# Performance work log

Hardware: AMD Instinct MI355X
Metric: run time of the kernel (lower is better)

Reference implementation:

```python
import jax, jax.numpy as jnp
import numpy as np

GRID_X, GRID_Y, GRID_Z = 200, 200, 8  # grid_size init kwarg (static)


def setup_inputs() -> dict:
    key = jax.random.key(0)
    k1, k2 = jax.random.split(key)
    B, N, D, H, W, C = 4, 6, 41, 16, 44, 64
    # ego-frame points roughly covering the grid extent [-50,50]x[-50,50]x[-4,4]
    scale = jnp.array([55.0, 55.0, 5.0], dtype=jnp.float32)
    geometry = jax.random.uniform(k1, (B, N, D, H, W, 3), dtype=jnp.float32,
                                  minval=-1.0, maxval=1.0) * scale
    features = jax.random.normal(k2, (B, N, D, H, W, C), dtype=jnp.float32)
    voxel_size = jnp.array([0.5, 0.5, 1.0], dtype=jnp.float32)
    voxel_origin = jnp.array([-50.0, -50.0, -4.0], dtype=jnp.float32)
    return {"geometry": geometry, "features": features,
            "voxel_size": voxel_size, "voxel_origin": voxel_origin}


def reference(geometry, features, voxel_size, voxel_origin):
    B = features.shape[0]
    C = features.shape[-1]
    pts = geometry.reshape(B, -1, 3)          # [B, P, 3]
    feat = features.reshape(B, -1, C)         # [B, P, C]

    # metric -> voxel index
    vi = jnp.floor((pts - voxel_origin) / voxel_size).astype(jnp.int32)  # [B, P, 3]
    x, y, z = vi[..., 0], vi[..., 1], vi[..., 2]
    valid = ((x >= 0) & (x < GRID_X) &
             (y >= 0) & (y < GRID_Y) &
             (z >= 0) & (z < GRID_Z))         # [B, P]

    # linear voxel index (z, x, y) ordering; invalid points scatter zeros to slot 0
    lin = z * (GRID_X * GRID_Y) + x * GRID_Y + y
    lin = jnp.where(valid, lin, 0)
    feat_m = jnp.where(valid[..., None], feat, 0.0)

    num_vox = GRID_Z * GRID_X * GRID_Y

    def pool_one(lin_b, feat_b):
        # scatter-add features into dense voxel grid: [num_vox, C]
        return jax.ops.segment_sum(feat_b, lin_b, num_segments=num_vox)

    vox = jax.vmap(pool_one)(lin, feat_m)                         # [B, num_vox, C]
    vox = vox.reshape(B, GRID_Z, GRID_X, GRID_Y, C)
    # torch.cat over z along channel dim => [B, Z*C, X, Y] with z-major blocks
    bev = jnp.transpose(vox, (0, 1, 4, 2, 3)).reshape(B, GRID_Z * C, GRID_X, GRID_Y)
    return bev
```

## Files before the change

kernel.cpp:

```cpp
#include <hip/hip_runtime.h>
#include <hip/hip_bf16.h>


#define GRID_X 200
#define GRID_Y 200
#define GRID_Z 8
#define NCH 64
#define NB 4
#define PTS_PER_BATCH (6 * 41 * 16 * 44)
#define TOTAL_POINTS (NB * PTS_PER_BATCH)
#define OUT_FLOATS ((long long)NB * GRID_Z * NCH * GRID_X * GRID_Y)

#define YT 2
#define TILE_Y 100
#define NBUCKET (NB * GRID_Z * GRID_X * YT)
#define LDS_STRIDE 65

#define WS_CNT     0
#define WS_STARTS  (NBUCKET)
#define WS_CURSOR  (2 * NBUCKET + 1)
#define WS_SORTED  (3 * NBUCKET + 1)
#define WS_PCODE   (3 * NBUCKET + 1 + TOTAL_POINTS)
#define WS_INTS    (3 * NBUCKET + 1 + 2 * TOTAL_POINTS)

__device__ __forceinline__ bool point_voxel(const float* __restrict__ geom,
                                            const float* __restrict__ vsz,
                                            const float* __restrict__ vorg,
                                            int i, int& vx, int& vy, int& vz) {
    float px = geom[(size_t)i * 3 + 0];
    float py = geom[(size_t)i * 3 + 1];
    float pz = geom[(size_t)i * 3 + 2];
    vx = (int)floorf((px - vorg[0]) / vsz[0]);
    vy = (int)floorf((py - vorg[1]) / vsz[1]);
    vz = (int)floorf((pz - vorg[2]) / vsz[2]);
    return (vx >= 0 && vx < GRID_X && vy >= 0 && vy < GRID_Y &&
            vz >= 0 && vz < GRID_Z);
}

__global__ __launch_bounds__(256) void zero_cnt_kernel(int* __restrict__ cnt) {
    int i = blockIdx.x * 256 + threadIdx.x;
    if (i < NBUCKET) cnt[i] = 0;
}

__global__ __launch_bounds__(256) void hist_kernel(
    const float* __restrict__ geom, const float* __restrict__ vsz,
    const float* __restrict__ vorg, int* __restrict__ cnt,
    unsigned* __restrict__ pcode) {
    int i = blockIdx.x * 256 + threadIdx.x;
    if (i >= TOTAL_POINTS) return;
    int vx, vy, vz;
    unsigned code = 0;
    if (point_voxel(geom, vsz, vorg, i, vx, vy, vz)) {
        int b = i / PTS_PER_BATCH;
        int yt = vy / TILE_Y;
        int yl = vy - yt * TILE_Y;
        int bucket = ((b * GRID_Z + vz) * GRID_X + vx) * YT + yt;
        code = 0x80000000u | ((unsigned)yl << 14) | (unsigned)bucket;
        atomicAdd(&cnt[bucket], 1);
    }
    pcode[i] = code;
}

__global__ __launch_bounds__(256) void scan_kernel(
    const int* __restrict__ cnt, int* __restrict__ starts, int* __restrict__ cursor) {
    __shared__ int partial[256];
    int t = threadIdx.x;
    const int CHUNK = NBUCKET / 256;
    int base = t * CHUNK;
    int s = 0;
    for (int j = 0; j < CHUNK; ++j) s += cnt[base + j];
    partial[t] = s;
    __syncthreads();
    for (int off = 1; off < 256; off <<= 1) {
        int v = (t >= off) ? partial[t - off] : 0;
        __syncthreads();
        partial[t] += v;
        __syncthreads();
    }
    int run = partial[t] - s;
    for (int j = 0; j < CHUNK; ++j) {
        int c = cnt[base + j];
        starts[base + j] = run;
        cursor[base + j] = run;
        run += c;
    }
    if (t == 255) starts[NBUCKET] = run;
}

__global__ __launch_bounds__(256) void scatter_idx_kernel(
    const unsigned* __restrict__ pcode, int* __restrict__ cursor,
    unsigned* __restrict__ sorted) {
    int i = blockIdx.x * 256 + threadIdx.x;
    if (i >= TOTAL_POINTS) return;
    unsigned code = pcode[i];
    if (!(code & 0x80000000u)) return;
    int bucket = (int)(code & 0x3FFFu);
    unsigned yl = (code >> 14) & 0x7Fu;
    int pos = atomicAdd(&cursor[bucket], 1);
    sorted[pos] = (unsigned)i | (yl << 20);
}

__global__ __launch_bounds__(256) void pool_kernel(
    const float4* __restrict__ feat4, const unsigned* __restrict__ sorted,
    const int* __restrict__ starts, float4* __restrict__ out4) {
    __shared__ __align__(16) float acc[TILE_Y * LDS_STRIDE];
    int t = threadIdx.x;
    int bid = blockIdx.x;

    float4* a4 = (float4*)acc;
    for (int i = t; i < TILE_Y * LDS_STRIDE / 4; i += 256)
        a4[i] = make_float4(0.f, 0.f, 0.f, 0.f);
    __syncthreads();

    int s0 = starts[bid];
    int s1 = starts[bid + 1];
    int w = t >> 6;
    int g = (t >> 4) & 3;
    int l = t & 15;

    for (int p0 = s0 + w * 4; p0 < s1; p0 += 16) {
        int p = p0 + g;
        if (p < s1) {
            unsigned pk = sorted[p];
            unsigned idx = pk & 0xFFFFFu;
            unsigned yl = pk >> 20;
            float4 f = feat4[(size_t)idx * 16 + l];
            float* row = &acc[yl * LDS_STRIDE + 4 * l];
            atomicAdd(row + 0, f.x);
            atomicAdd(row + 1, f.y);
            atomicAdd(row + 2, f.z);
            atomicAdd(row + 3, f.w);
        }
    }
    __syncthreads();

    int yt = bid & 1;
    int x = (bid >> 1) % GRID_X;
    int bz = (bid >> 1) / GRID_X;

    for (int i = t; i < NCH * (TILE_Y / 4); i += 256) {
        int cc = i / (TILE_Y / 4);
        int j = i % (TILE_Y / 4);
        int y0 = 4 * j;
        float4 v = make_float4(acc[(y0 + 0) * LDS_STRIDE + cc],
                               acc[(y0 + 1) * LDS_STRIDE + cc],
                               acc[(y0 + 2) * LDS_STRIDE + cc],
                               acc[(y0 + 3) * LDS_STRIDE + cc]);
        size_t o4 = (((size_t)bz * NCH + cc) * GRID_X + x) * (GRID_Y / 4)
                    + yt * (TILE_Y / 4) + j;
        out4[o4] = v;
    }
}

__global__ __launch_bounds__(256) void zero_out_kernel(float4* __restrict__ out) {
    const long long n4 = OUT_FLOATS / 4;
    long long stride = (long long)gridDim.x * blockDim.x;
    for (long long i = blockIdx.x * (long long)blockDim.x + threadIdx.x;
         i < n4; i += stride)
        out[i] = make_float4(0.f, 0.f, 0.f, 0.f);
}

__global__ __launch_bounds__(256) void voxel_scatter_kernel(
    const float* __restrict__ geom, const float* __restrict__ feat,
    const float* __restrict__ vsz, const float* __restrict__ vorg,
    float* __restrict__ out) {
    int gid = blockIdx.x * blockDim.x + threadIdx.x;
    int pt = gid >> 6;
    int c = gid & 63;
    if (pt >= TOTAL_POINTS) return;
    int vx, vy, vz;
    if (!point_voxel(geom, vsz, vorg, pt, vx, vy, vz)) return;
    int b = pt / PTS_PER_BATCH;
    float f = feat[(size_t)pt * NCH + c];
    size_t idx = ((((size_t)b * GRID_Z + vz) * NCH + c) * GRID_X + vx) * GRID_Y + vy;
    atomicAdd(out + idx, f);
}

extern "C" void kernel_launch(void* const* d_in, const int* in_sizes, int n_in,
                              void* d_out, int out_size, void* d_ws, size_t ws_size,
                              hipStream_t stream) {
    const float* geom = (const float*)d_in[0];
    const float* feat = (const float*)d_in[1];
    const float* vsz  = (const float*)d_in[2];
    const float* vorg = (const float*)d_in[3];
    float* out = (float*)d_out;

    if (ws_size >= (size_t)WS_INTS * sizeof(int)) {
        int* ws = (int*)d_ws;
        int* cnt = ws + WS_CNT;
        int* starts = ws + WS_STARTS;
        int* cursor = ws + WS_CURSOR;
        unsigned* sorted = (unsigned*)(ws + WS_SORTED);
        unsigned* pcode  = (unsigned*)(ws + WS_PCODE);

        zero_cnt_kernel<<<(NBUCKET + 255) / 256, 256, 0, stream>>>(cnt);
        hist_kernel<<<TOTAL_POINTS / 256, 256, 0, stream>>>(geom, vsz, vorg, cnt, pcode);
        scan_kernel<<<1, 256, 0, stream>>>(cnt, starts, cursor);
        scatter_idx_kernel<<<TOTAL_POINTS / 256, 256, 0, stream>>>(pcode, cursor, sorted);
        pool_kernel<<<NBUCKET, 256, 0, stream>>>(
            (const float4*)feat, sorted, starts, (float4*)out);
    } else {
        zero_out_kernel<<<2048, 256, 0, stream>>>((float4*)out);
        const long long total_threads = (long long)TOTAL_POINTS * NCH;
        voxel_scatter_kernel<<<(int)((total_threads + 255) / 256), 256, 0, stream>>>(
            geom, feat, vsz, vorg, out);
    }
}
```

Before: 600.7 us.

## Regroup pooling buckets by x-groups with channel slices and y-contiguous LDS tiles

Bucketing changes from (x, y-half) tiles to groups of 4 x-columns covering the full y range. Each pool block now handles a 16-channel slice with an LDS accumulator laid out channel/x-major and y-contiguous. The write-out reads contiguous y values from LDS and issues nontemporal vector stores to the output. Each point's bucket is now read by 4 blocks (one per channel slice), so sorted indices and codes are re-read, while each feature load is narrower.

```diff
diff --git a/kernel.cpp b/kernel.cpp
--- a/kernel.cpp
+++ b/kernel.cpp
@@ -1,5 +1,4 @@
 #include <hip/hip_runtime.h>
-#include <hip/hip_bf16.h>
 
 
 #define GRID_X 200
@@ -11,17 +10,22 @@
 #define TOTAL_POINTS (NB * PTS_PER_BATCH)
 #define OUT_FLOATS ((long long)NB * GRID_Z * NCH * GRID_X * GRID_Y)
 
-#define YT 2
-#define TILE_Y 100
-#define NBUCKET (NB * GRID_Z * GRID_X * YT)
-#define LDS_STRIDE 65
+#define XG 4
+#define NXG (GRID_X / XG)
+#define CS 16
+#define NSLICE (NCH / CS)
+#define NBUCK (NB * GRID_Z * NXG)
+#define YSTRIDE 201
+#define ACC_FLOATS (CS * XG * YSTRIDE)
+
+typedef float nt4 __attribute__((ext_vector_type(4)));
 
 #define WS_CNT     0
-#define WS_STARTS  (NBUCKET)
-#define WS_CURSOR  (2 * NBUCKET + 1)
-#define WS_SORTED  (3 * NBUCKET + 1)
-#define WS_PCODE   (3 * NBUCKET + 1 + TOTAL_POINTS)
-#define WS_INTS    (3 * NBUCKET + 1 + 2 * TOTAL_POINTS)
+#define WS_STARTS  (NBUCK)
+#define WS_CURSOR  (2 * NBUCK + 1)
+#define WS_SORTED  (3 * NBUCK + 1)
+#define WS_PCODE   (3 * NBUCK + 1 + TOTAL_POINTS)
+#define WS_INTS    (3 * NBUCK + 1 + 2 * TOTAL_POINTS)
 
 __device__ __forceinline__ bool point_voxel(const float* __restrict__ geom,
                                             const float* __restrict__ vsz,
@@ -39,7 +43,7 @@
 
 __global__ __launch_bounds__(256) void zero_cnt_kernel(int* __restrict__ cnt) {
     int i = blockIdx.x * 256 + threadIdx.x;
-    if (i < NBUCKET) cnt[i] = 0;
+    if (i < NBUCK) cnt[i] = 0;
 }
 
 __global__ __launch_bounds__(256) void hist_kernel(
@@ -52,10 +56,9 @@
     unsigned code = 0;
     if (point_voxel(geom, vsz, vorg, i, vx, vy, vz)) {
         int b = i / PTS_PER_BATCH;
-        int yt = vy / TILE_Y;
-        int yl = vy - yt * TILE_Y;
-        int bucket = ((b * GRID_Z + vz) * GRID_X + vx) * YT + yt;
-        code = 0x80000000u | ((unsigned)yl << 14) | (unsigned)bucket;
+        int bucket = (b * GRID_Z + vz) * NXG + (vx >> 2);
+        code = 0x80000000u | ((unsigned)vy << 13) |
+               ((unsigned)(vx & 3) << 11) | (unsigned)bucket;
         atomicAdd(&cnt[bucket], 1);
     }
     pcode[i] = code;
@@ -65,10 +68,13 @@
     const int* __restrict__ cnt, int* __restrict__ starts, int* __restrict__ cursor) {
     __shared__ int partial[256];
     int t = threadIdx.x;
-    const int CHUNK = NBUCKET / 256;
+    const int CHUNK = (NBUCK + 255) / 256;
     int base = t * CHUNK;
     int s = 0;
-    for (int j = 0; j < CHUNK; ++j) s += cnt[base + j];
+    for (int j = 0; j < CHUNK; ++j) {
+        int k = base + j;
+        if (k < NBUCK) s += cnt[k];
+    }
     partial[t] = s;
     __syncthreads();
     for (int off = 1; off < 256; off <<= 1) {
@@ -79,12 +85,15 @@
     }
     int run = partial[t] - s;
     for (int j = 0; j < CHUNK; ++j) {
-        int c = cnt[base + j];
-        starts[base + j] = run;
-        cursor[base + j] = run;
-        run += c;
-    }
-    if (t == 255) starts[NBUCKET] = run;
+        int k = base + j;
+        if (k < NBUCK) {
+            int c = cnt[k];
+            starts[k] = run;
+            cursor[k] = run;
+            run += c;
+        }
+    }
+    if (t == 255) starts[NBUCK] = partial[255];
 }
 
 __global__ __launch_bounds__(256) void scatter_idx_kernel(
@@ -94,61 +103,68 @@
     if (i >= TOTAL_POINTS) return;
     unsigned code = pcode[i];
     if (!(code & 0x80000000u)) return;
-    int bucket = (int)(code & 0x3FFFu);
-    unsigned yl = (code >> 14) & 0x7Fu;
+    int bucket = (int)(code & 0x7FFu);
+    unsigned xl = (code >> 11) & 3u;
+    unsigned yl = (code >> 13) & 0xFFu;
     int pos = atomicAdd(&cursor[bucket], 1);
-    sorted[pos] = (unsigned)i | (yl << 20);
+    sorted[pos] = (unsigned)i | (xl << 20) | (yl << 22);
 }
 
 __global__ __launch_bounds__(256) void pool_kernel(
     const float4* __restrict__ feat4, const unsigned* __restrict__ sorted,
-    const int* __restrict__ starts, float4* __restrict__ out4) {
-    __shared__ __align__(16) float acc[TILE_Y * LDS_STRIDE];
+    const int* __restrict__ starts, float* __restrict__ out) {
+    __shared__ __align__(16) float acc[ACC_FLOATS];
     int t = threadIdx.x;
     int bid = blockIdx.x;
+    int cs = bid & (NSLICE - 1);
+    int bucket = bid >> 2;
 
     float4* a4 = (float4*)acc;
-    for (int i = t; i < TILE_Y * LDS_STRIDE / 4; i += 256)
+    for (int i = t; i < ACC_FLOATS / 4; i += 256)
         a4[i] = make_float4(0.f, 0.f, 0.f, 0.f);
     __syncthreads();
 
-    int s0 = starts[bid];
-    int s1 = starts[bid + 1];
+    int s0 = starts[bucket];
+    int s1 = starts[bucket + 1];
     int w = t >> 6;
-    int g = (t >> 4) & 3;
-    int l = t & 15;
-
-    for (int p0 = s0 + w * 4; p0 < s1; p0 += 16) {
+    int g = (t >> 2) & 15;
+    int l = t & 3;
+
+    for (int p0 = s0 + w * 16; p0 < s1; p0 += 64) {
         int p = p0 + g;
         if (p < s1) {
             unsigned pk = sorted[p];
             unsigned idx = pk & 0xFFFFFu;
-            unsigned yl = pk >> 20;
-            float4 f = feat4[(size_t)idx * 16 + l];
-            float* row = &acc[yl * LDS_STRIDE + 4 * l];
-            atomicAdd(row + 0, f.x);
-            atomicAdd(row + 1, f.y);
-            atomicAdd(row + 2, f.z);
-            atomicAdd(row + 3, f.w);
+            int xl = (int)((pk >> 20) & 3u);
+            int yl = (int)(pk >> 22);
+            float4 f = feat4[(size_t)idx * (NCH / 4) + cs * (CS / 4) + l];
+            int cb = 4 * l;
+            atomicAdd(&acc[((cb + 0) * XG + xl) * YSTRIDE + yl], f.x);
+            atomicAdd(&acc[((cb + 1) * XG + xl) * YSTRIDE + yl], f.y);
+            atomicAdd(&acc[((cb + 2) * XG + xl) * YSTRIDE + yl], f.z);
+            atomicAdd(&acc[((cb + 3) * XG + xl) * YSTRIDE + yl], f.w);
         }
     }
     __syncthreads();
 
-    int yt = bid & 1;
-    int x = (bid >> 1) % GRID_X;
-    int bz = (bid >> 1) / GRID_X;
-
-    for (int i = t; i < NCH * (TILE_Y / 4); i += 256) {
-        int cc = i / (TILE_Y / 4);
-        int j = i % (TILE_Y / 4);
+    int xg = bucket % NXG;
+    int bz = bucket / NXG;
+    int x0 = xg * XG;
+
+    nt4* out4 = (nt4*)out;
+    for (int i = t; i < CS * XG * (GRID_Y / 4); i += 256) {
+        int j = i % (GRID_Y / 4);
+        int cx = i / (GRID_Y / 4);
         int y0 = 4 * j;
-        float4 v = make_float4(acc[(y0 + 0) * LDS_STRIDE + cc],
-                               acc[(y0 + 1) * LDS_STRIDE + cc],
-                               acc[(y0 + 2) * LDS_STRIDE + cc],
-                               acc[(y0 + 3) * LDS_STRIDE + cc]);
-        size_t o4 = (((size_t)bz * NCH + cc) * GRID_X + x) * (GRID_Y / 4)
-                    + yt * (TILE_Y / 4) + j;
-        out4[o4] = v;
+        nt4 v = {acc[cx * YSTRIDE + y0 + 0],
+                 acc[cx * YSTRIDE + y0 + 1],
+                 acc[cx * YSTRIDE + y0 + 2],
+                 acc[cx * YSTRIDE + y0 + 3]};
+        int xl = cx & 3;
+        int cl = cx >> 2;
+        int cc = cs * CS + cl;
+        size_t o4 = (((size_t)bz * NCH + cc) * GRID_X + (x0 + xl)) * (GRID_Y / 4) + j;
+        __builtin_nontemporal_store(v, &out4[o4]);
     }
 }
 
@@ -193,12 +209,12 @@
         unsigned* sorted = (unsigned*)(ws + WS_SORTED);
         unsigned* pcode  = (unsigned*)(ws + WS_PCODE);
 
-        zero_cnt_kernel<<<(NBUCKET + 255) / 256, 256, 0, stream>>>(cnt);
+        zero_cnt_kernel<<<(NBUCK + 255) / 256, 256, 0, stream>>>(cnt);
         hist_kernel<<<TOTAL_POINTS / 256, 256, 0, stream>>>(geom, vsz, vorg, cnt, pcode);
         scan_kernel<<<1, 256, 0, stream>>>(cnt, starts, cursor);
         scatter_idx_kernel<<<TOTAL_POINTS / 256, 256, 0, stream>>>(pcode, cursor, sorted);
-        pool_kernel<<<NBUCKET, 256, 0, stream>>>(
-            (const float4*)feat, sorted, starts, (float4*)out);
+        pool_kernel<<<NBUCK * NSLICE, 256, 0, stream>>>(
+            (const float4*)feat, sorted, starts, out);
     } else {
         zero_out_kernel<<<2048, 256, 0, stream>>>((float4*)out);
         const long long total_threads = (long long)TOTAL_POINTS * NCH;
```

Measured after the change: 716.0 us. 1.19x slower.
